# Kernel tuning notes

Hardware: AMD Instinct MI355X
Metric: run time of the kernel (lower is better)

The kernel has to match this reference:

```python
import jax, jax.numpy as jnp
import numpy as np

NUM_BITS_ACTS = 8
NUM_BITS_PARAMS = 8
NUM_BITS_ACCUM = 32


def quantized_range(num_bits):
    # distiller-style signed range: [-2^(n-1), 2^(n-1)-1]
    n = 2.0 ** num_bits
    return -n / 2.0, n / 2.0 - 1.0


def sym_scale(num_bits, sat_abs):
    # scale = (2^(n-1)-1) / max_abs
    return (2.0 ** (num_bits - 1) - 1.0) / sat_abs


def quant_clamp(t, scale, qmin, qmax):
    return jnp.clip(jnp.round(t * scale), qmin, qmax)


def setup_inputs() -> dict:
    key = jax.random.key(0)
    kx, kw = jax.random.split(key)
    x = jax.random.normal(kx, (8192, 4096), dtype=jnp.float32)
    W = jax.random.normal(kw, (4096, 4096), dtype=jnp.float32)  # [out, in]
    return {"x": x, "W": W}


def reference(x, W):
    acts_min, acts_max = quantized_range(NUM_BITS_ACTS)
    params_min, params_max = quantized_range(NUM_BITS_PARAMS)
    accum_min, accum_max = quantized_range(NUM_BITS_ACCUM)

    # __init__: quantize weights once (symmetric, max-abs)
    w_scale = sym_scale(NUM_BITS_PARAMS, jnp.max(jnp.abs(W)))
    W_q = quant_clamp(W, w_scale, params_min, params_max)

    # pre_quantized_forward: input scale from max-abs, quantize-clamp input
    in_scale = sym_scale(NUM_BITS_ACTS, jnp.max(jnp.abs(x)))
    x_q = quant_clamp(x, in_scale, acts_min, acts_max)

    # wrapped Linear in integer domain, clamp to accumulator range
    accum = jnp.clip(x_q @ W_q.T, accum_min, accum_max)  # [8192, 4096]

    # post_quantized_forward: requantize accumulator to output range
    accum_scale = in_scale * w_scale
    accum_max_abs = jnp.max(jnp.abs(accum))
    y_f_max_abs = accum_max_abs / accum_scale
    out_scale = sym_scale(NUM_BITS_ACTS, y_f_max_abs)
    requant_scale = out_scale / accum_scale

    out_q = quant_clamp(accum, requant_scale, acts_min, acts_max)
    out_f = out_q / out_scale  # dequantize
    return out_f
```

## Files before the change

### kernel.cpp

```cpp
#include <hip/hip_runtime.h>
#include <stdint.h>


using i32x4 = __attribute__((ext_vector_type(4))) int;

#define M_DIM 8192
#define N_DIM 4096
#define K_DIM 4096

#define BM 256
#define BN 256
#define BKB 128
#define NKT (K_DIM / BKB)

__global__ void k_init(unsigned* sc) {
    sc[0] = 0u;
    sc[1] = 0u;
    sc[2] = 0u;
}

__global__ __launch_bounds__(256) void k_absmax2(const float4* __restrict__ x,
                                                 const float4* __restrict__ w,
                                                 unsigned* __restrict__ sc) {
    const bool isX = blockIdx.x < 2048;
    const float4* src = isX ? x : w;
    const int n4 = isX ? (M_DIM * K_DIM / 4) : (N_DIM * K_DIM / 4);
    const int brel = isX ? blockIdx.x : (blockIdx.x - 2048);
    const int nb = isX ? 2048 : 1024;
    unsigned m = 0;
    for (int i = brel * 256 + threadIdx.x; i < n4; i += nb * 256) {
        float4 v = src[i];
        unsigned a = __float_as_uint(v.x) & 0x7fffffffu;
        unsigned b = __float_as_uint(v.y) & 0x7fffffffu;
        unsigned c = __float_as_uint(v.z) & 0x7fffffffu;
        unsigned d = __float_as_uint(v.w) & 0x7fffffffu;
        m = max(m, max(max(a, b), max(c, d)));
    }
    for (int off = 32; off; off >>= 1)
        m = max(m, (unsigned)__shfl_xor((int)m, off));
    __shared__ unsigned wm[4];
    int ln = threadIdx.x & 63, wv = threadIdx.x >> 6;
    if (ln == 0) wm[wv] = m;
    __syncthreads();
    if (threadIdx.x == 0)
        atomicMax(sc + (isX ? 0 : 1), max(max(wm[0], wm[1]), max(wm[2], wm[3])));
}

__global__ __launch_bounds__(256) void k_quant2(const float4* __restrict__ x,
                                                const float4* __restrict__ w,
                                                unsigned* __restrict__ xq,
                                                unsigned* __restrict__ wq,
                                                const unsigned* __restrict__ sc) {
    const bool isX = blockIdx.x < 2048;
    const float4* src = isX ? x : w;
    unsigned* dst = isX ? xq : wq;
    const int n4 = isX ? (M_DIM * K_DIM / 4) : (N_DIM * K_DIM / 4);
    const int brel = isX ? blockIdx.x : (blockIdx.x - 2048);
    const int nb = isX ? 2048 : 1024;
    const float scale = 127.0f / __uint_as_float(sc[isX ? 0 : 1]);
    for (int i = brel * 256 + threadIdx.x; i < n4; i += nb * 256) {
        float4 v = src[i];
        int q0 = min(127, max(-128, (int)rintf(v.x * scale)));
        int q1 = min(127, max(-128, (int)rintf(v.y * scale)));
        int q2 = min(127, max(-128, (int)rintf(v.z * scale)));
        int q3 = min(127, max(-128, (int)rintf(v.w * scale)));
        dst[i] = (unsigned)(q0 & 0xff) | ((unsigned)(q1 & 0xff) << 8) |
                 ((unsigned)(q2 & 0xff) << 16) | ((unsigned)(q3 & 0xff) << 24);
    }
}

__global__ __launch_bounds__(512, 2) void k_gemm(const char* __restrict__ Aq,
                                                 const char* __restrict__ Bq,
                                                 int* __restrict__ C,
                                                 unsigned* __restrict__ maxAcc) {
    __shared__ __align__(16) char lds[131072];
    __shared__ int wmax[8];

    const int t = threadIdx.x;
    const int ln = t & 63;
    const int wv = t >> 6;
    const int wr = wv >> 2;
    const int wc = wv & 3;
    const int lr = ln & 15;
    const int lk = ln >> 4;

    const int bid = blockIdx.x;
    const int swz = (bid & 7) * 64 + (bid >> 3);
    const int bx = swz & 15;
    const int by = swz >> 4;
    const int arow0 = by * BM;
    const int brow0 = bx * BN;

    const int cs0 = lk ^ (lr & 7);
    const int aoff0 = (((wr << 7) + lr) << 7) + (cs0 << 4);
    const int aoff1 = aoff0 ^ 64;
    const int boff0 = (((wc << 6) + lr) << 7) + (cs0 << 4);
    const int boff1 = boff0 ^ 64;

    int voffA[2], voffB[2];
#pragma unroll
    for (int it = 0; it < 2; ++it) {
        const int chunk = it * 512 + (wv << 6) + ln;
        const int row = chunk >> 3;
        const int gc = (chunk & 7) ^ (row & 7);
        voffA[it] = (arow0 + row) * 4096 + (gc << 4);
        voffB[it] = (brow0 + row) * 4096 + (gc << 4);
    }

    i32x4 acc[8][4];
#pragma unroll
    for (int i = 0; i < 8; ++i)
#pragma unroll
        for (int j = 0; j < 4; ++j) acc[i][j] = (i32x4)(0);

    auto STAGE = [&](int kt, int j) {
        const int slot = kt & 1;
        const int koff = kt * 128 + (j & 1) * 524288;
        const bool isA = (j < 2);
        const char* gbase = isA ? Aq : Bq;
        const int* voff = isA ? voffA : voffB;
        char* lbase = lds + (isA ? 0 : 65536) + (slot << 15) + ((j & 1) << 14) + (wv << 10);
#pragma unroll
        for (int it = 0; it < 2; ++it) {
            const char* g = gbase + (unsigned)(voff[it] + koff);
            __builtin_amdgcn_global_load_lds(
                (const __attribute__((address_space(1))) void*)g,
                (__attribute__((address_space(3))) void*)(lbase + (it << 13)), 16, 0, 0);
        }
    };

    STAGE(0, 0); STAGE(0, 1); STAGE(0, 2); STAGE(0, 3);
    STAGE(1, 2); STAGE(1, 3);
    asm volatile("s_waitcnt vmcnt(4)" ::: "memory");
    __builtin_amdgcn_s_barrier();
    __builtin_amdgcn_sched_barrier(0);

    for (int kt = 0; kt < NKT; ++kt) {
        const int sl = (kt & 1) << 15;
        const char* pA0 = lds + sl + aoff0;
        const char* pA1 = lds + sl + aoff1;
        const char* pB0 = lds + 65536 + sl + boff0;
        const char* pB1 = lds + 65536 + sl + boff1;
        i32x4 a[4][2], b[4][2];

#pragma unroll
        for (int mi = 0; mi < 4; ++mi) {
            a[mi][0] = *(const i32x4*)(pA0 + (mi << 11));
            a[mi][1] = *(const i32x4*)(pA1 + (mi << 11));
        }
#pragma unroll
        for (int ni = 0; ni < 4; ++ni) {
            b[ni][0] = *(const i32x4*)(pB0 + (ni << 11));
            b[ni][1] = *(const i32x4*)(pB1 + (ni << 11));
        }
        if (kt + 1 < NKT) { STAGE(kt + 1, 0); STAGE(kt + 1, 1); }
        __builtin_amdgcn_s_setprio(1);
#pragma unroll
        for (int kh = 0; kh < 2; ++kh)
#pragma unroll
            for (int mi = 0; mi < 4; ++mi)
#pragma unroll
                for (int ni = 0; ni < 4; ++ni)
                    acc[mi][ni] = __builtin_amdgcn_mfma_i32_16x16x64_i8(
                        a[mi][kh], b[ni][kh], acc[mi][ni], 0, 0, 0);
        __builtin_amdgcn_s_setprio(0);
#pragma unroll
        for (int mi = 0; mi < 4; ++mi) {
            a[mi][0] = *(const i32x4*)(pA0 + ((mi + 4) << 11));
            a[mi][1] = *(const i32x4*)(pA1 + ((mi + 4) << 11));
        }
        __builtin_amdgcn_s_barrier();
        __builtin_amdgcn_sched_barrier(0);

        if (kt + 2 < NKT) {
            STAGE(kt + 2, 2); STAGE(kt + 2, 3);
            asm volatile("s_waitcnt vmcnt(4)" ::: "memory");
        } else {
            asm volatile("s_waitcnt vmcnt(0)" ::: "memory");
        }
        __builtin_amdgcn_s_setprio(1);
#pragma unroll
        for (int kh = 0; kh < 2; ++kh)
#pragma unroll
            for (int mi = 0; mi < 4; ++mi)
#pragma unroll
                for (int ni = 0; ni < 4; ++ni)
                    acc[mi + 4][ni] = __builtin_amdgcn_mfma_i32_16x16x64_i8(
                        a[mi][kh], b[ni][kh], acc[mi + 4][ni], 0, 0, 0);
        __builtin_amdgcn_s_setprio(0);
        __builtin_amdgcn_s_barrier();
        __builtin_amdgcn_sched_barrier(0);
    }

    int amax = 0;
#pragma unroll
    for (int mi = 0; mi < 8; ++mi) {
#pragma unroll
        for (int ni = 0; ni < 4; ++ni) {
            const int row0 = arow0 + (wr << 7) + (mi << 4) + (lk << 2);
            const int col  = brow0 + (wc << 6) + (ni << 4) + lr;
            i32x4 v = acc[mi][ni];
#pragma unroll
            for (int j = 0; j < 4; ++j) {
                C[(size_t)(row0 + j) * N_DIM + col] = v[j];
                int a = v[j] < 0 ? -v[j] : v[j];
                amax = max(amax, a);
            }
        }
    }
    for (int off = 32; off; off >>= 1)
        amax = max(amax, __shfl_xor(amax, off));
    if (ln == 0) wmax[wv] = amax;
    __syncthreads();
    if (t == 0) {
        int m = wmax[0];
#pragma unroll
        for (int i = 1; i < 8; ++i) m = max(m, wmax[i]);
        atomicMax(maxAcc, (unsigned)m);
    }
}

__global__ __launch_bounds__(256) void k_requant(int4* __restrict__ buf, int n4,
                                                 const unsigned* __restrict__ sc) {
    const float maxX = __uint_as_float(sc[0]);
    const float maxW = __uint_as_float(sc[1]);
    const float maxA = (float)(int)sc[2];
    const float in_scale = 127.0f / maxX;
    const float w_scale  = 127.0f / maxW;
    const float accum_scale = in_scale * w_scale;
    const float requant = 127.0f / maxA;
    const float out_scale = requant * accum_scale;
    int stride = gridDim.x * blockDim.x;
    for (int i = blockIdx.x * blockDim.x + threadIdx.x; i < n4; i += stride) {
        int4 v = buf[i];
        float4 o;
        o.x = fminf(127.f, fmaxf(-128.f, rintf((float)v.x * requant))) / out_scale;
        o.y = fminf(127.f, fmaxf(-128.f, rintf((float)v.y * requant))) / out_scale;
        o.z = fminf(127.f, fmaxf(-128.f, rintf((float)v.z * requant))) / out_scale;
        o.w = fminf(127.f, fmaxf(-128.f, rintf((float)v.w * requant))) / out_scale;
        ((float4*)buf)[i] = o;
    }
}

extern "C" void kernel_launch(void* const* d_in, const int* in_sizes, int n_in,
                              void* d_out, int out_size, void* d_ws, size_t ws_size,
                              hipStream_t stream) {
    const float* x = (const float*)d_in[0];
    const float* W = (const float*)d_in[1];

    unsigned* sc = (unsigned*)d_ws;
    char* xq = (char*)d_ws + 256;
    char* wq = xq + (size_t)M_DIM * K_DIM;

    k_init<<<1, 1, 0, stream>>>(sc);
    k_absmax2<<<3072, 256, 0, stream>>>((const float4*)x, (const float4*)W, sc);
    k_quant2<<<3072, 256, 0, stream>>>((const float4*)x, (const float4*)W,
                                       (unsigned*)xq, (unsigned*)wq, sc);
    k_gemm<<<(M_DIM / BM) * (N_DIM / BN), 512, 0, stream>>>(xq, wq, (int*)d_out, sc + 2);
    k_requant<<<2048, 256, 0, stream>>>((int4*)d_out, M_DIM * N_DIM / 4, sc);
}
```

Before: 282.0 us.

## Widen quant stores to 16 bytes, reorder GEMM barrier, use memset for init

```diff
diff --git a/kernel.cpp b/kernel.cpp
--- a/kernel.cpp
+++ b/kernel.cpp
@@ -12,12 +12,6 @@
 #define BN 256
 #define BKB 128
 #define NKT (K_DIM / BKB)
-
-__global__ void k_init(unsigned* sc) {
-    sc[0] = 0u;
-    sc[1] = 0u;
-    sc[2] = 0u;
-}
 
 __global__ __launch_bounds__(256) void k_absmax2(const float4* __restrict__ x,
                                                  const float4* __restrict__ w,
@@ -48,24 +42,34 @@
 
 __global__ __launch_bounds__(256) void k_quant2(const float4* __restrict__ x,
                                                 const float4* __restrict__ w,
-                                                unsigned* __restrict__ xq,
-                                                unsigned* __restrict__ wq,
+                                                uint4* __restrict__ xq,
+                                                uint4* __restrict__ wq,
                                                 const unsigned* __restrict__ sc) {
     const bool isX = blockIdx.x < 2048;
     const float4* src = isX ? x : w;
-    unsigned* dst = isX ? xq : wq;
-    const int n4 = isX ? (M_DIM * K_DIM / 4) : (N_DIM * K_DIM / 4);
+    uint4* dst = isX ? xq : wq;
+    const int n16 = (isX ? (M_DIM * K_DIM) : (N_DIM * K_DIM)) / 16;
     const int brel = isX ? blockIdx.x : (blockIdx.x - 2048);
     const int nb = isX ? 2048 : 1024;
     const float scale = 127.0f / __uint_as_float(sc[isX ? 0 : 1]);
-    for (int i = brel * 256 + threadIdx.x; i < n4; i += nb * 256) {
-        float4 v = src[i];
+
+    auto pack = [&](float4 v) -> unsigned {
         int q0 = min(127, max(-128, (int)rintf(v.x * scale)));
         int q1 = min(127, max(-128, (int)rintf(v.y * scale)));
         int q2 = min(127, max(-128, (int)rintf(v.z * scale)));
         int q3 = min(127, max(-128, (int)rintf(v.w * scale)));
-        dst[i] = (unsigned)(q0 & 0xff) | ((unsigned)(q1 & 0xff) << 8) |
-                 ((unsigned)(q2 & 0xff) << 16) | ((unsigned)(q3 & 0xff) << 24);
+        return (unsigned)(q0 & 0xff) | ((unsigned)(q1 & 0xff) << 8) |
+               ((unsigned)(q2 & 0xff) << 16) | ((unsigned)(q3 & 0xff) << 24);
+    };
+
+    for (int i = brel * 256 + threadIdx.x; i < n16; i += nb * 256) {
+        const float4* s = src + i * 4;
+        uint4 o;
+        o.x = pack(s[0]);
+        o.y = pack(s[1]);
+        o.z = pack(s[2]);
+        o.w = pack(s[3]);
+        dst[i] = o;
     }
 }
 
@@ -164,14 +168,14 @@
                     acc[mi][ni] = __builtin_amdgcn_mfma_i32_16x16x64_i8(
                         a[mi][kh], b[ni][kh], acc[mi][ni], 0, 0, 0);
         __builtin_amdgcn_s_setprio(0);
+        __builtin_amdgcn_s_barrier();
+        __builtin_amdgcn_sched_barrier(0);
+
 #pragma unroll
         for (int mi = 0; mi < 4; ++mi) {
             a[mi][0] = *(const i32x4*)(pA0 + ((mi + 4) << 11));
             a[mi][1] = *(const i32x4*)(pA1 + ((mi + 4) << 11));
         }
-        __builtin_amdgcn_s_barrier();
-        __builtin_amdgcn_sched_barrier(0);
-
         if (kt + 2 < NKT) {
             STAGE(kt + 2, 2); STAGE(kt + 2, 3);
             asm volatile("s_waitcnt vmcnt(4)" ::: "memory");
@@ -252,10 +256,10 @@
     char* xq = (char*)d_ws + 256;
     char* wq = xq + (size_t)M_DIM * K_DIM;
 
-    k_init<<<1, 1, 0, stream>>>(sc);
+    hipMemsetAsync(sc, 0, 16, stream);
     k_absmax2<<<3072, 256, 0, stream>>>((const float4*)x, (const float4*)W, sc);
     k_quant2<<<3072, 256, 0, stream>>>((const float4*)x, (const float4*)W,
-                                       (unsigned*)xq, (unsigned*)wq, sc);
+                                       (uint4*)xq, (uint4*)wq, sc);
     k_gemm<<<(M_DIM / BM) * (N_DIM / BN), 512, 0, stream>>>(xq, wq, (int*)d_out, sc + 2);
     k_requant<<<2048, 256, 0, stream>>>((int4*)d_out, M_DIM * N_DIM / 4, sc);
 }
```

Result: faster. 272.2 us (-3.5%).
